# Optimization experiments

Hardware: AMD Instinct MI355X
Metric: run time of the kernel (lower is better)

The kernel has to match this reference:

```python
import jax, jax.numpy as jnp
import numpy as np

B, DIM, H, W = 64, 384, 28, 28
NH, HD, WS, SS = 6, 64, 7, 3
HID = 1536
N = WS * WS
NW = (H // WS) * (W // WS)
SCALE = HD ** -0.25  # qk_scale=None -> head_dim ** -0.25, applied to both q and k
EPS = 1e-5


def _rel_pos_index(ws):
    coords = np.stack(np.meshgrid(np.arange(ws), np.arange(ws), indexing='ij'))  # (2,ws,ws)
    flat = coords.reshape(2, -1)
    rel = (flat[:, :, None] - flat[:, None, :]).transpose(1, 2, 0).copy()  # (N,N,2)
    rel[..., 0] += ws - 1
    rel[..., 1] += ws - 1
    rel[..., 0] *= 2 * ws - 1
    return rel.sum(-1)  # (N,N) int


def _attn_mask(h, w, ws, ss):
    img = np.zeros((h, w))
    cnt = 0
    for hs in (slice(0, -ws), slice(-ws, -ss), slice(-ss, None)):
        for wsl in (slice(0, -ws), slice(-ws, -ss), slice(-ss, None)):
            img[hs, wsl] = cnt
            cnt += 1
    mw = img.reshape(h // ws, ws, w // ws, ws).transpose(0, 2, 1, 3).reshape(-1, ws * ws)  # (nW,N)
    diff = mw[:, None, :] - mw[:, :, None]
    return np.where(diff != 0, -100.0, 0.0).astype(np.float32)  # (nW,N,N)


REL_IDX = jnp.asarray(_rel_pos_index(WS))          # (N,N)
MASK = jnp.asarray(_attn_mask(H, W, WS, SS))       # (NW,N,N)


def _layernorm_bchw(x, w, b):
    mean = jnp.mean(x, axis=1, keepdims=True)
    var = jnp.var(x, axis=1, keepdims=True, ddof=1)  # torch.var_mean is unbiased
    return (x - mean) / jnp.sqrt(var + EPS) * w + b


def setup_inputs() -> dict:
    key = jax.random.key(0)
    ks = jax.random.split(key, 6)
    return {
        'x': jax.random.normal(ks[0], (B, DIM, H, W), jnp.float32),
        'norm1_w': jnp.ones((1, DIM, 1, 1), jnp.float32),
        'norm1_b': jnp.zeros((1, DIM, 1, 1), jnp.float32),
        'qkv_w': jax.random.normal(ks[1], (3 * NH * HD, DIM), jnp.float32) * 0.02,
        'rel_bias_table': jax.random.normal(ks[2], ((2 * WS - 1) ** 2, NH), jnp.float32) * 0.02,
        'proj_w': jax.random.normal(ks[3], (DIM, NH * HD), jnp.float32) * 0.02,
        'norm2_w': jnp.ones((1, DIM, 1, 1), jnp.float32),
        'norm2_b': jnp.zeros((1, DIM, 1, 1), jnp.float32),
        'mlp_w1': jax.random.normal(ks[4], (HID, DIM), jnp.float32) * 0.02,
        'mlp_w3': jax.random.normal(ks[5], (DIM, HID), jnp.float32) * 0.02,
    }


def reference(x, norm1_w, norm1_b, qkv_w, rel_bias_table, proj_w, norm2_w, norm2_b, mlp_w1, mlp_w3):
    b = x.shape[0]
    shortcut = x
    xn = _layernorm_bchw(x, norm1_w, norm1_b)
    xs = jnp.roll(xn, (-SS, -SS), axis=(2, 3))
    # window partition: (B,C,H,W) -> (B*nW, C, WS, WS)
    xw = xs.reshape(b, DIM, H // WS, WS, W // WS, WS).transpose(0, 2, 4, 1, 3, 5).reshape(-1, DIM, WS, WS)
    bw = xw.shape[0]
    # 1x1-conv qkv projection (no bias), then split heads
    qkv = jnp.einsum('oc,bchw->bohw', qkv_w, xw).reshape(bw, 3, NH, HD, N)
    q, k, v = jnp.moveaxis(qkv, 1, 0)  # each (bw, NH, HD, N)
    attn = jnp.einsum('bhdn,bhdm->bhnm', q * SCALE, k * SCALE)  # (bw,NH,N,N)
    bias = rel_bias_table[REL_IDX.reshape(-1)].reshape(N, N, NH).transpose(2, 0, 1)  # (NH,N,N)
    attn = attn + bias[None]
    attn = attn.reshape(b, NW, NH, N, N) + MASK[None, :, None]
    attn = jax.nn.softmax(attn.reshape(bw, NH, N, N), axis=-1)
    out = jnp.einsum('bhnm,bhdm->bhdn', attn, v)  # (bw,NH,HD,N)
    out = out.reshape(bw, NH * HD, WS, WS)
    out = jnp.einsum('oc,bchw->bohw', proj_w, out)
    # window reverse + unshift
    xr = out.reshape(b, H // WS, W // WS, DIM, WS, WS).transpose(0, 3, 1, 4, 2, 5).reshape(b, DIM, H, W)
    xr = jnp.roll(xr, (SS, SS), axis=(2, 3))
    x = shortcut + xr
    # conv MLP (1x1 convs, no bias, exact GELU)
    xn2 = _layernorm_bchw(x, norm2_w, norm2_b)
    h = jax.nn.gelu(jnp.einsum('oc,bchw->bohw', mlp_w1, xn2), approximate=False)
    x = x + jnp.einsum('oc,bchw->bohw', mlp_w3, h)
    return x
```

## Files before the change

kernel.cpp:

```cpp
#include <hip/hip_runtime.h>
#include <hip/hip_bf16.h>


typedef __bf16 bf16x8 __attribute__((ext_vector_type(8)));
typedef __bf16 bf16x4 __attribute__((ext_vector_type(4)));
typedef float  f32x4  __attribute__((ext_vector_type(4)));
typedef float  f32x2  __attribute__((ext_vector_type(2)));
typedef int    i32x4  __attribute__((ext_vector_type(4)));
typedef int    i32x2  __attribute__((ext_vector_type(2)));

#define GAS __attribute__((address_space(1)))
#define LAS __attribute__((address_space(3)))

#if __has_builtin(__builtin_amdgcn_cvt_pk_f32_fp8) && __has_builtin(__builtin_amdgcn_cvt_pk_fp8_f32)
#define HAS_HW_FP8 1
#else
#define HAS_HW_FP8 0
#endif

__device__ __forceinline__ int div7u(int m) { return (m * 37) >> 8; }

#if !HAS_HW_FP8
__device__ __forceinline__ float fp8_dec1(unsigned u) {
  unsigned s = (u >> 7) & 1, e = (u >> 3) & 15, m = u & 7;
  float nrm = __uint_as_float((s << 31) | ((e + 120) << 23) | (m << 20));
  float sub = (s ? -1.f : 1.f) * (float)m * 0.001953125f;
  return e ? nrm : sub;
}
__device__ __forceinline__ unsigned fp8_enc1(float f) {
  f = fminf(fmaxf(f, -448.f), 448.f);
  unsigned u = __float_as_uint(f);
  unsigned s = u >> 31;
  int e8 = (int)((u >> 23) & 255) - 120;
  unsigned m32 = u & 0x7fffff;
  if (e8 <= 0) return s << 7;
  unsigned m = m32 >> 20;
  unsigned rem = m32 & 0xfffff;
  m += (rem > 0x80000u) || (rem == 0x80000u && (m & 1));
  if (m == 8) { m = 0; ++e8; }
  if (e8 > 15 || (e8 == 15 && m == 7)) { e8 = 15; m = 6; }
  return (s << 7) | ((unsigned)e8 << 3) | m;
}
#endif

template <bool HI>
__device__ __forceinline__ f32x2 fp8_cvt2(int w) {
#if HAS_HW_FP8
  return __builtin_amdgcn_cvt_pk_f32_fp8(w, HI);
#else
  unsigned b0 = (w >> (HI ? 16 : 0)) & 255, b1 = (w >> (HI ? 24 : 8)) & 255;
  return (f32x2){fp8_dec1(b0), fp8_dec1(b1)};
#endif
}
template <bool HI>
__device__ __forceinline__ int fp8_pk2(float a, float b, int old) {
#if HAS_HW_FP8
  return __builtin_amdgcn_cvt_pk_fp8_f32(a, b, old, HI);
#else
  unsigned v = fp8_enc1(a) | (fp8_enc1(b) << 8);
  return HI ? (int)(((unsigned)old & 0xffffu) | (v << 16))
            : (int)(((unsigned)old & 0xffff0000u) | v);
#endif
}
__device__ __forceinline__ i32x4 fp8x8_to_bf16x8(i32x2 v) {
  f32x2 a = fp8_cvt2<false>(v[0]), b = fp8_cvt2<true>(v[0]);
  f32x2 c = fp8_cvt2<false>(v[1]), d = fp8_cvt2<true>(v[1]);
  bf16x8 r = {(__bf16)a[0], (__bf16)a[1], (__bf16)b[0], (__bf16)b[1],
              (__bf16)c[0], (__bf16)c[1], (__bf16)d[0], (__bf16)d[1]};
  return __builtin_bit_cast(i32x4, r);
}

__device__ __forceinline__ float gelu_f(float v) {
  float u = v * __builtin_fmaf(0.0356774f, v * v, 0.79788456f);
  float e = __expf(2.f * u);
  float t = 1.f - 2.f * __builtin_amdgcn_rcpf(e + 1.f);
  return 0.5f * v * (1.f + t);
}

__global__ __launch_bounds__(256) void cvt_all_kernel(const float* __restrict__ s0,
                                                      const float* __restrict__ s1,
                                                      const float* __restrict__ s2,
                                                      const float* __restrict__ s3,
                                                      __bf16* __restrict__ d0,
                                                      __bf16* __restrict__ d1,
                                                      __bf16* __restrict__ d2,
                                                      __bf16* __restrict__ d3,
                                                      const float* __restrict__ tbl,
                                                      float* __restrict__ be) {
  int i = blockIdx.x * 256 + threadIdx.x;
  if (i < 442368) { d0[i] = (__bf16)s0[i]; return; }
  i -= 442368;
  if (i < 147456) { d1[i] = (__bf16)s1[i]; return; }
  i -= 147456;
  if (i < 589824) { d2[i] = (__bf16)s2[i]; return; }
  i -= 589824;
  if (i < 589824) { d3[i] = (__bf16)s3[i]; return; }
  i -= 589824;
  if (i < 6 * 64 * 64) {
    int m = i & 63, n = (i >> 6) & 63, h = i >> 12;
    float v = 0.f;
    if (m < 49 && n < 49) {
      int in_ = div7u(n), jn = n - in_ * 7;
      int im  = div7u(m), jm = m - im * 7;
      v = tbl[((in_ - im + 6) * 13 + (jn - jm + 6)) * 6 + h];
    }
    be[i] = v;
  }
}

__global__ __launch_bounds__(256) void ln_t_kernel(const float* __restrict__ x,
                                                   const float* __restrict__ gw,
                                                   const float* __restrict__ gb,
                                                   __bf16* __restrict__ out) {
  __shared__ f32x4 ps[16][16], ps2[16][16];
  __shared__ __align__(16) __bf16 tile[64][198];
  const int tid = threadIdx.x;
  const int lane = tid & 63, w = tid >> 6;
  const int gq = lane & 15;
  const int sub = (w << 2) + (lane >> 4);
  const int tok0 = blockIdx.x << 6;
  const int tokg4 = tok0 + (gq << 2);
  const unsigned b = (unsigned)tokg4 / 784u;
  const unsigned p = (unsigned)tokg4 - b * 784u;
  const float* xp = x + (size_t)b * 301056u + p;

  f32x4 vals[24];
  f32x4 s4 = {0.f, 0.f, 0.f, 0.f}, s24 = {0.f, 0.f, 0.f, 0.f};
  #pragma unroll
  for (int half = 0; half < 2; ++half)
    #pragma unroll
    for (int k = 0; k < 12; ++k) {
      int c = half * 192 + sub * 12 + k;
      f32x4 v = *(const f32x4*)(xp + (size_t)c * 784u);
      vals[half * 12 + k] = v;
      s4 += v;
      s24 += v * v;
    }
  ps[sub][gq] = s4;
  ps2[sub][gq] = s24;
  __syncthreads();
  f32x4 S = {0.f, 0.f, 0.f, 0.f}, S2 = {0.f, 0.f, 0.f, 0.f};
  #pragma unroll
  for (int i = 0; i < 16; ++i) { S += ps[i][gq]; S2 += ps2[i][gq]; }
  f32x4 mean = S * (1.f / 384.f);
  f32x4 var = (S2 - S * mean) * (1.f / 383.f);
  f32x4 rstd;
  #pragma unroll
  for (int j = 0; j < 4; ++j) rstd[j] = rsqrtf(var[j] + 1e-5f);

  #pragma unroll
  for (int half = 0; half < 2; ++half) {
    if (half) __syncthreads();
    #pragma unroll
    for (int k = 0; k < 12; ++k) {
      int c = half * 192 + sub * 12 + k;
      float wgt = gw[c], bia = gb[c];
      f32x4 v = (vals[half * 12 + k] - mean) * rstd * wgt + bia;
      #pragma unroll
      for (int j = 0; j < 4; ++j)
        tile[(gq << 2) + j][sub * 12 + k] = (__bf16)v[j];
    }
    __syncthreads();
    #pragma unroll
    for (int it = 0; it < 6; ++it) {
      int idx = (it << 8) + tid;
      int row = idx / 24, colc = idx - row * 24;
      bf16x8 vv = *(const bf16x8*)(&tile[row][colc << 3]);
      *(bf16x8*)(out + (size_t)(tok0 + row) * 384 + half * 192 + (colc << 3)) = vv;
    }
  }
}

template <int EPI, int F8>
__global__ __launch_bounds__(256, 3) void gemm_bt(const __bf16* __restrict__ A, int lda,
                                                  const void* __restrict__ BtV, int ldb,
                                                  int K, int My,
                                                  void* __restrict__ outT, int ldo, int ocol,
                                                  float* __restrict__ outR,
                                                  const float* __restrict__ resid,
                                                  int tok_off) {
  constexpr bool B8 = (F8 && EPI == 2);
  constexpr int esz = B8 ? 1 : 2;
  __shared__ __align__(16) char smem[33792];
  const int tid = threadIdx.x;
  const int lane = tid & 63;
  const int w = tid >> 6;
  const int wr = w >> 1, wc = w & 1;
  const int c = lane & 15, g = lane >> 4;

  const int nwg = gridDim.x;
  const int orig = blockIdx.x;
  const int q = nwg >> 3, r = nwg & 7;
  const int xcd = orig & 7, ii = orig >> 3;
  const int wgid = (xcd < r ? xcd * (q + 1) : r * (q + 1) + (xcd - r) * q) + ii;
  const int bx = wgid / My;
  const int by = wgid - bx * My;
  const int m0 = by << 7;
  const int n0 = bx << 7;

  const __bf16* ap[4];
  const unsigned char* bp[4];
  #pragma unroll
  for (int i = 0; i < 4; ++i) {
    int s = (i << 8) + tid;
    int row = s >> 3;
    int kk = ((s ^ row) & 7) << 3;
    ap[i] = A + (size_t)(m0 + row) * lda + kk;
    bp[i] = (const unsigned char*)BtV + ((size_t)(n0 + row) * ldb + kk) * esz;
  }

  i32x4 sA0, sA1, sA2, sA3;
  i32x4 sB0, sB1, sB2, sB3;
  i32x2 t0, t1, t2, t3;
  auto issue = [&](int k0) {
    sA0 = *(const i32x4*)(ap[0] + k0);
    sA1 = *(const i32x4*)(ap[1] + k0);
    sA2 = *(const i32x4*)(ap[2] + k0);
    sA3 = *(const i32x4*)(ap[3] + k0);
    if constexpr (B8) {
      t0 = *(const i32x2*)(bp[0] + k0);
      t1 = *(const i32x2*)(bp[1] + k0);
      t2 = *(const i32x2*)(bp[2] + k0);
      t3 = *(const i32x2*)(bp[3] + k0);
    } else {
      sB0 = *(const i32x4*)(bp[0] + k0 * 2);
      sB1 = *(const i32x4*)(bp[1] + k0 * 2);
      sB2 = *(const i32x4*)(bp[2] + k0 * 2);
      sB3 = *(const i32x4*)(bp[3] + k0 * 2);
    }
  };
  auto write_lds = [&]() {
    *(i32x4*)(smem +         (((0 << 8) + tid) << 4)) = sA0;
    *(i32x4*)(smem +         (((1 << 8) + tid) << 4)) = sA1;
    *(i32x4*)(smem +         (((2 << 8) + tid) << 4)) = sA2;
    *(i32x4*)(smem +         (((3 << 8) + tid) << 4)) = sA3;
    if constexpr (B8) {
      *(i32x4*)(smem + 16384 + (((0 << 8) + tid) << 4)) = fp8x8_to_bf16x8(t0);
      *(i32x4*)(smem + 16384 + (((1 << 8) + tid) << 4)) = fp8x8_to_bf16x8(t1);
      *(i32x4*)(smem + 16384 + (((2 << 8) + tid) << 4)) = fp8x8_to_bf16x8(t2);
      *(i32x4*)(smem + 16384 + (((3 << 8) + tid) << 4)) = fp8x8_to_bf16x8(t3);
    } else {
      *(i32x4*)(smem + 16384 + (((0 << 8) + tid) << 4)) = sB0;
      *(i32x4*)(smem + 16384 + (((1 << 8) + tid) << 4)) = sB1;
      *(i32x4*)(smem + 16384 + (((2 << 8) + tid) << 4)) = sB2;
      *(i32x4*)(smem + 16384 + (((3 << 8) + tid) << 4)) = sB3;
    }
  };

  f32x4 acc[4][4] = {};
  const int nt = K >> 6;

  issue(0);
  write_lds();
  asm volatile("s_waitcnt lgkmcnt(0)" ::: "memory");
  __builtin_amdgcn_s_barrier();
  __builtin_amdgcn_sched_barrier(0);

  for (int t = 0; t < nt; ++t) {
    if (t + 1 < nt) issue((t + 1) << 6);
    const char* smA = smem;
    const char* smB = smem + 16384;
    #pragma unroll
    for (int ks = 0; ks < 2; ++ks) {
      bf16x8 af[4], bfv[4];
      #pragma unroll
      for (int mi = 0; mi < 4; ++mi) {
        int r2 = (wr << 6) + (mi << 4) + c;
        af[mi] = *(const bf16x8*)(smA + (r2 << 7) + (((ks << 6) + (g << 4)) ^ ((r2 & 7) << 4)));
      }
      #pragma unroll
      for (int nj = 0; nj < 4; ++nj) {
        int r2 = (wc << 6) + (nj << 4) + c;
        bfv[nj] = *(const bf16x8*)(smB + (r2 << 7) + (((ks << 6) + (g << 4)) ^ ((r2 & 7) << 4)));
      }
      #pragma unroll
      for (int mi = 0; mi < 4; ++mi)
        #pragma unroll
        for (int nj = 0; nj < 4; ++nj) {
          if constexpr (EPI == 2)
            acc[mi][nj] = __builtin_amdgcn_mfma_f32_16x16x32_bf16(bfv[nj], af[mi], acc[mi][nj], 0, 0, 0);
          else
            acc[mi][nj] = __builtin_amdgcn_mfma_f32_16x16x32_bf16(af[mi], bfv[nj], acc[mi][nj], 0, 0, 0);
        }
    }
    __builtin_amdgcn_s_barrier();
    if (t + 1 < nt) {
      write_lds();
      asm volatile("s_waitcnt lgkmcnt(0)" ::: "memory");
    }
    __builtin_amdgcn_s_barrier();
    __builtin_amdgcn_sched_barrier(0);
  }

  if constexpr (EPI <= 1) {
    #pragma unroll
    for (int mi = 0; mi < 4; ++mi)
      #pragma unroll
      for (int nj = 0; nj < 4; ++nj) {
        f32x4 v = acc[mi][nj];
        if constexpr (EPI == 1) {
          #pragma unroll
          for (int r2 = 0; r2 < 4; ++r2) v[r2] = gelu_f(v[r2]);
        }
        bf16x4 pk = {(__bf16)v[0], (__bf16)v[1], (__bf16)v[2], (__bf16)v[3]};
        int nl = (wc << 6) + (nj << 4) + c;
        int ml = (wr << 6) + (mi << 4) + (g << 2);
        *(bf16x4*)(smem + nl * 264 + ml * 2) = pk;
      }
    __syncthreads();
    #pragma unroll
    for (int it = 0; it < 8; ++it) {
      int id = (it << 8) + tid;
      int n = id >> 4, mc = id & 15;
      bf16x8 v = *(const bf16x8*)(smem + n * 264 + (mc << 4));
      if constexpr (F8) {
        int w0 = 0, w1 = 0;
        w0 = fp8_pk2<false>((float)v[0], (float)v[1], w0);
        w0 = fp8_pk2<true>((float)v[2], (float)v[3], w0);
        w1 = fp8_pk2<false>((float)v[4], (float)v[5], w1);
        w1 = fp8_pk2<true>((float)v[6], (float)v[7], w1);
        *(i32x2*)((unsigned char*)outT + (size_t)(n0 + n) * ldo + (ocol + m0 + (mc << 3))) =
            (i32x2){w0, w1};
      } else {
        *(bf16x8*)((__bf16*)outT + (size_t)(n0 + n) * ldo + (ocol + m0 + (mc << 3))) = v;
      }
    }
  } else {
    #pragma unroll
    for (int nj = 0; nj < 4; ++nj) {
      int tokb = tok_off + n0 + (wc << 6) + (nj << 4) + (g << 2);
      unsigned bb = (unsigned)tokb / 784u;
      unsigned pp = (unsigned)tokb - bb * 784u;
      size_t base2 = (size_t)bb * (384u * 784u) + pp;
      #pragma unroll
      for (int mi = 0; mi < 4; ++mi) {
        int o = m0 + (wr << 6) + (mi << 4) + c;
        size_t a2 = base2 + (size_t)o * 784u;
        f32x4 rv = *(const f32x4*)(resid + a2);
        f32x4 v = acc[mi][nj] + rv;
        *(f32x4*)(outR + a2) = v;
      }
    }
  }
}

__global__ __launch_bounds__(256, 2) void attn_kernel(const __bf16* __restrict__ qkv,
                                                      const float* __restrict__ be,
                                                      __bf16* __restrict__ outt) {
  __shared__ __align__(16) char smem_all[4][16384];
  const int tid = threadIdx.x;
  const int lane = tid & 63;
  const int w = tid >> 6;
  char* sm = (char*)smem_all[w];
  const int pair = blockIdx.x * 4 + w;
  const int h = pair % 6;
  const int wg = pair / 6;
  const int b = wg >> 4;
  const int wi = wg & 15;
  const int wh = wi >> 2, wwi = wi & 3;
  const int cc = lane & 15, g = lane >> 4;

  {
    int rsub = lane >> 3;
    int slot = lane & 7;
    int dc = (slot ^ rsub) << 3;
    #pragma unroll
    for (int i = 0; i < 8; ++i) {
      int r = i * 8 + rsub;
      int m = r < 49 ? r : 48;
      int im = div7u(m), jm = m - im * 7;
      int sh = wh * 7 + im + 3; if (sh >= 28) sh -= 28;
      int sw = wwi * 7 + jm + 3; if (sw >= 28) sw -= 28;
      size_t trow = (size_t)(b * 784 + sh * 28 + sw) * 1152;
      __builtin_amdgcn_global_load_lds((const GAS void*)(qkv + trow + 384 + h * 64 + dc),
                                       (LAS void*)(sm + i * 1024), 16, 0, 0);
      __builtin_amdgcn_global_load_lds((const GAS void*)(qkv + trow + h * 64 + dc),
                                       (LAS void*)(sm + 8192 + i * 1024), 16, 0, 0);
    }
  }
  asm volatile("s_waitcnt vmcnt(0)" ::: "memory");
  __syncthreads();

  f32x4 sacc[4][4] = {};
  #pragma unroll
  for (int ks = 0; ks < 2; ++ks) {
    bf16x8 kf[4], qf[4];
    #pragma unroll
    for (int mi = 0; mi < 4; ++mi) {
      int r = (mi << 4) + cc;
      kf[mi] = *(const bf16x8*)(sm + (r << 7) + (((ks << 6) + (g << 4)) ^ ((r & 7) << 4)));
    }
    #pragma unroll
    for (int nj = 0; nj < 4; ++nj) {
      int r = (nj << 4) + cc;
      qf[nj] = *(const bf16x8*)(sm + 8192 + (r << 7) + (((ks << 6) + (g << 4)) ^ ((r & 7) << 4)));
    }
    #pragma unroll
    for (int mi = 0; mi < 4; ++mi)
      #pragma unroll
      for (int nj = 0; nj < 4; ++nj)
        sacc[mi][nj] = __builtin_amdgcn_mfma_f32_16x16x32_bf16(kf[mi], qf[nj], sacc[mi][nj], 0, 0, 0);
  }
  __syncthreads();

  int r9m[4][4];
  #pragma unroll
  for (int mi = 0; mi < 4; ++mi)
    #pragma unroll
    for (int rr = 0; rr < 4; ++rr) {
      int m = (mi << 4) + (g << 2) + rr; if (m > 48) m = 48;
      int im = div7u(m), jm = m - im * 7;
      int sh = wh * 7 + im, sw = wwi * 7 + jm;
      r9m[mi][rr] = ((sh < 21) ? 0 : (sh < 25 ? 1 : 2)) * 3 + ((sw < 21) ? 0 : (sw < 25 ? 1 : 2));
    }

  #pragma unroll
  for (int nj = 0; nj < 4; ++nj) {
    int n = (nj << 4) + cc;
    int ncl = n > 48 ? 48 : n;
    int in_ = div7u(ncl), jn = ncl - in_ * 7;
    int shn = wh * 7 + in_, swn = wwi * 7 + jn;
    int r9n = ((shn < 21) ? 0 : (shn < 25 ? 1 : 2)) * 3 + ((swn < 21) ? 0 : (swn < 25 ? 1 : 2));
    float mx = -1e30f;
    #pragma unroll
    for (int mi = 0; mi < 4; ++mi) {
      f32x4 bia = *(const f32x4*)(be + (((h << 6) + n) << 6) + (mi << 4) + (g << 2));
      #pragma unroll
      for (int rr = 0; rr < 4; ++rr) {
        int m = (mi << 4) + (g << 2) + rr;
        float t = (m < 49)
            ? sacc[mi][nj][rr] * 0.125f + bia[rr] + ((r9m[mi][rr] == r9n) ? 0.f : -100.f)
            : -1e30f;
        sacc[mi][nj][rr] = t;
        mx = fmaxf(mx, t);
      }
    }
    mx = fmaxf(mx, __shfl_xor(mx, 16, 64));
    mx = fmaxf(mx, __shfl_xor(mx, 32, 64));
    float sum = 0.f;
    #pragma unroll
    for (int mi = 0; mi < 4; ++mi)
      #pragma unroll
      for (int rr = 0; rr < 4; ++rr) {
        float e = __expf(sacc[mi][nj][rr] - mx);
        sacc[mi][nj][rr] = e;
        sum += e;
      }
    sum += __shfl_xor(sum, 16, 64);
    sum += __shfl_xor(sum, 32, 64);
    float inv = __builtin_amdgcn_rcpf(sum);
    #pragma unroll
    for (int mi = 0; mi < 4; ++mi) {
      bf16x4 pk = {(__bf16)(sacc[mi][nj][0] * inv), (__bf16)(sacc[mi][nj][1] * inv),
                   (__bf16)(sacc[mi][nj][2] * inv), (__bf16)(sacc[mi][nj][3] * inv)};
      *(bf16x4*)(sm + 8192 + (n << 7) + (((mi << 5) + (g << 3)) ^ ((n & 7) << 4))) = pk;
    }
  }

  {
    int ml = lane & 15, dq = lane >> 4;
    #pragma unroll
    for (int it = 0; it < 4; ++it) {
      int m = (it << 4) + ml;
      int mc_ = m > 48 ? 48 : m;
      int im = div7u(mc_), jm = mc_ - im * 7;
      int sh = wh * 7 + im + 3; if (sh >= 28) sh -= 28;
      int sw = wwi * 7 + jm + 3; if (sw >= 28) sw -= 28;
      const __bf16* gv = qkv + (size_t)(b * 784 + sh * 28 + sw) * 1152 + 768 + h * 64;
      #pragma unroll
      for (int hd = 0; hd < 2; ++hd) {
        int dbase = (hd << 5) + (dq << 3);
        bf16x8 v = *(const bf16x8*)(gv + dbase);
        #pragma unroll
        for (int j = 0; j < 8; ++j) {
          int d = dbase + j;
          *(__bf16*)(sm + (d << 7) + ((((m >> 3) ^ (d & 7)) << 4) + ((m & 7) << 1))) = v[j];
        }
      }
    }
  }
  __syncthreads();

  f32x4 oacc[4][4] = {};
  #pragma unroll
  for (int ks = 0; ks < 2; ++ks) {
    bf16x8 pf[4], vf[4];
    #pragma unroll
    for (int ni = 0; ni < 4; ++ni) {
      int n = (ni << 4) + cc;
      pf[ni] = *(const bf16x8*)(sm + 8192 + (n << 7) + (((ks << 6) + (g << 4)) ^ ((n & 7) << 4)));
    }
    #pragma unroll
    for (int dj = 0; dj < 4; ++dj) {
      int d = (dj << 4) + cc;
      vf[dj] = *(const bf16x8*)(sm + (d << 7) + ((((ks << 2) + g) ^ (d & 7)) << 4));
    }
    #pragma unroll
    for (int ni = 0; ni < 4; ++ni)
      #pragma unroll
      for (int dj = 0; dj < 4; ++dj)
        oacc[ni][dj] = __builtin_amdgcn_mfma_f32_16x16x32_bf16(pf[ni], vf[dj], oacc[ni][dj], 0, 0, 0);
  }

  #pragma unroll
  for (int ni = 0; ni < 4; ++ni)
    #pragma unroll
    for (int rr = 0; rr < 4; ++rr) {
      int n = (ni << 4) + (g << 2) + rr;
      if (n < 49) {
        int im = div7u(n), jn = n - im * 7;
        int sh = wh * 7 + im + 3; if (sh >= 28) sh -= 28;
        int sw = wwi * 7 + jn + 3; if (sw >= 28) sw -= 28;
        __bf16* op = outt + (size_t)(b * 784 + sh * 28 + sw) * 384 + h * 64;
        #pragma unroll
        for (int dj = 0; dj < 4; ++dj)
          op[(dj << 4) + cc] = (__bf16)oacc[ni][dj][rr];
      }
    }
}

extern "C" void kernel_launch(void* const* d_in, const int* in_sizes, int n_in,
                              void* d_out, int out_size, void* d_ws, size_t ws_size,
                              hipStream_t stream) {
  (void)in_sizes; (void)n_in; (void)out_size; (void)ws_size;
  const float* x     = (const float*)d_in[0];
  const float* n1w   = (const float*)d_in[1];
  const float* n1b   = (const float*)d_in[2];
  const float* qkvw  = (const float*)d_in[3];
  const float* tbl   = (const float*)d_in[4];
  const float* projw = (const float*)d_in[5];
  const float* n2w   = (const float*)d_in[6];
  const float* n2b   = (const float*)d_in[7];
  const float* w1    = (const float*)d_in[8];
  const float* w3    = (const float*)d_in[9];
  float* out = (float*)d_out;

  char* ws = (char*)d_ws;
  __bf16* bufA = (__bf16*)ws;
  __bf16* bufB = (__bf16*)(ws + 38535168);
  float*  be   = (float*)(ws + 154140672);
  __bf16* wq   = (__bf16*)(ws + 154238976);
  __bf16* wp   = wq + 442368;
  __bf16* wm1  = wp + 147456;
  __bf16* wm3  = wm1 + 589824;

  cvt_all_kernel<<<7008, 256, 0, stream>>>(qkvw, projw, w1, w3, wq, wp, wm1, wm3, tbl, be);

  ln_t_kernel<<<784, 256, 0, stream>>>(x, n1w, n1b, bufA);
  gemm_bt<0, 0><<<392 * 9, 256, 0, stream>>>(wq, 384, bufA, 384, 384, 9,
                                             bufB, 1152, 0, nullptr, nullptr, 0);
  attn_kernel<<<1536, 256, 0, stream>>>(bufB, be, bufA);
  gemm_bt<2, 0><<<392 * 3, 256, 0, stream>>>(wp, 384, bufA, 384, 384, 3,
                                             nullptr, 0, 0, out, x, 0);
  ln_t_kernel<<<784, 256, 0, stream>>>(out, n2w, n2b, bufA);
  unsigned char* h8 = (unsigned char*)bufB;
  for (int hh = 0; hh < 2; ++hh) {
    const int toff = hh * 25088;
    gemm_bt<1, 1><<<196 * 12, 256, 0, stream>>>(wm1, 384, bufA + (size_t)toff * 384, 384, 384, 12,
                                                (void*)h8, 1536, 0, nullptr, nullptr, 0);
    gemm_bt<2, 1><<<196 * 3, 256, 0, stream>>>(wm3, 1536, (const void*)h8, 1536, 1536, 3,
                                               nullptr, 0, 0, out, out, toff);
  }
}
```

Before: 392.5 us.

## Add LDS-free direct-load GEMM with 128x256 tiles for qkv and MLP1

```diff
diff --git a/kernel.cpp b/kernel.cpp
--- a/kernel.cpp
+++ b/kernel.cpp
@@ -171,16 +171,95 @@
   }
 }
 
-template <int EPI, int F8>
+template <int EPI>
+__global__ __launch_bounds__(256, 2) void gemm_l2(const __bf16* __restrict__ A,
+                                                  const __bf16* __restrict__ Bt, int ldb,
+                                                  int My,
+                                                  void* __restrict__ outT, int ldo) {
+  __shared__ __align__(16) char smem[67584];
+  const int tid = threadIdx.x;
+  const int lane = tid & 63;
+  const int w = tid >> 6;
+  const int wr = w >> 1, wc = w & 1;
+  const int c = lane & 15, g = lane >> 4;
+
+  const int nwg = gridDim.x;
+  const int orig = blockIdx.x;
+  const int q = nwg >> 3, r = nwg & 7;
+  const int xcd = orig & 7, ii = orig >> 3;
+  const int wgid = (xcd < r ? xcd * (q + 1) : r * (q + 1) + (xcd - r) * q) + ii;
+  const int bx = wgid / My;
+  const int by = wgid - bx * My;
+  const int m0 = by << 7;
+  const int n0 = bx << 8;
+
+  const __bf16* aP = A + (size_t)(m0 + (wr << 6) + c) * 384 + (g << 3);
+  const __bf16* bP = Bt + (size_t)(n0 + (wc << 7) + c) * ldb + (g << 3);
+
+  f32x4 acc[4][8];
+  #pragma unroll
+  for (int mi = 0; mi < 4; ++mi)
+    #pragma unroll
+    for (int nj = 0; nj < 8; ++nj) acc[mi][nj] = (f32x4){0.f, 0.f, 0.f, 0.f};
+
+  #pragma unroll
+  for (int kk = 0; kk < 12; ++kk) {
+    bf16x8 af[4], bfv[8];
+    #pragma unroll
+    for (int mi = 0; mi < 4; ++mi)
+      af[mi] = *(const bf16x8*)(aP + (mi << 4) * 384 + (kk << 5));
+    #pragma unroll
+    for (int nj = 0; nj < 8; ++nj)
+      bfv[nj] = *(const bf16x8*)(bP + (size_t)((nj << 4)) * ldb + (kk << 5));
+    #pragma unroll
+    for (int mi = 0; mi < 4; ++mi)
+      #pragma unroll
+      for (int nj = 0; nj < 8; ++nj)
+        acc[mi][nj] = __builtin_amdgcn_mfma_f32_16x16x32_bf16(af[mi], bfv[nj], acc[mi][nj], 0, 0, 0);
+  }
+
+  #pragma unroll
+  for (int mi = 0; mi < 4; ++mi)
+    #pragma unroll
+    for (int nj = 0; nj < 8; ++nj) {
+      f32x4 v = acc[mi][nj];
+      if constexpr (EPI == 1) {
+        #pragma unroll
+        for (int j = 0; j < 4; ++j) v[j] = gelu_f(v[j]);
+      }
+      bf16x4 pk = {(__bf16)v[0], (__bf16)v[1], (__bf16)v[2], (__bf16)v[3]};
+      int tok = (wc << 7) + (nj << 4) + c;
+      int ml = (wr << 6) + (mi << 4) + (g << 2);
+      *(bf16x4*)(smem + tok * 264 + ml * 2) = pk;
+    }
+  __syncthreads();
+  #pragma unroll
+  for (int it = 0; it < 16; ++it) {
+    int id = (it << 8) + tid;
+    int n = id >> 4, mc = id & 15;
+    bf16x8 v = *(const bf16x8*)(smem + n * 264 + (mc << 4));
+    if constexpr (EPI == 1) {
+      int w0 = 0, w1 = 0;
+      w0 = fp8_pk2<false>((float)v[0], (float)v[1], w0);
+      w0 = fp8_pk2<true>((float)v[2], (float)v[3], w0);
+      w1 = fp8_pk2<false>((float)v[4], (float)v[5], w1);
+      w1 = fp8_pk2<true>((float)v[6], (float)v[7], w1);
+      *(i32x2*)((unsigned char*)outT + (size_t)(n0 + n) * ldo + (m0 + (mc << 3))) =
+          (i32x2){w0, w1};
+    } else {
+      *(bf16x8*)((__bf16*)outT + (size_t)(n0 + n) * ldo + (m0 + (mc << 3))) = v;
+    }
+  }
+}
+
+template <int F8>
 __global__ __launch_bounds__(256, 3) void gemm_bt(const __bf16* __restrict__ A, int lda,
                                                   const void* __restrict__ BtV, int ldb,
                                                   int K, int My,
-                                                  void* __restrict__ outT, int ldo, int ocol,
                                                   float* __restrict__ outR,
                                                   const float* __restrict__ resid,
                                                   int tok_off) {
-  constexpr bool B8 = (F8 && EPI == 2);
-  constexpr int esz = B8 ? 1 : 2;
+  constexpr int esz = F8 ? 1 : 2;
   __shared__ __align__(16) char smem[33792];
   const int tid = threadIdx.x;
   const int lane = tid & 63;
@@ -217,7 +296,7 @@
     sA1 = *(const i32x4*)(ap[1] + k0);
     sA2 = *(const i32x4*)(ap[2] + k0);
     sA3 = *(const i32x4*)(ap[3] + k0);
-    if constexpr (B8) {
+    if constexpr (F8) {
       t0 = *(const i32x2*)(bp[0] + k0);
       t1 = *(const i32x2*)(bp[1] + k0);
       t2 = *(const i32x2*)(bp[2] + k0);
@@ -234,7 +313,7 @@
     *(i32x4*)(smem +         (((1 << 8) + tid) << 4)) = sA1;
     *(i32x4*)(smem +         (((2 << 8) + tid) << 4)) = sA2;
     *(i32x4*)(smem +         (((3 << 8) + tid) << 4)) = sA3;
-    if constexpr (B8) {
+    if constexpr (F8) {
       *(i32x4*)(smem + 16384 + (((0 << 8) + tid) << 4)) = fp8x8_to_bf16x8(t0);
       *(i32x4*)(smem + 16384 + (((1 << 8) + tid) << 4)) = fp8x8_to_bf16x8(t1);
       *(i32x4*)(smem + 16384 + (((2 << 8) + tid) << 4)) = fp8x8_to_bf16x8(t2);
@@ -276,12 +355,8 @@
       #pragma unroll
       for (int mi = 0; mi < 4; ++mi)
         #pragma unroll
-        for (int nj = 0; nj < 4; ++nj) {
-          if constexpr (EPI == 2)
-            acc[mi][nj] = __builtin_amdgcn_mfma_f32_16x16x32_bf16(bfv[nj], af[mi], acc[mi][nj], 0, 0, 0);
-          else
-            acc[mi][nj] = __builtin_amdgcn_mfma_f32_16x16x32_bf16(af[mi], bfv[nj], acc[mi][nj], 0, 0, 0);
-        }
+        for (int nj = 0; nj < 4; ++nj)
+          acc[mi][nj] = __builtin_amdgcn_mfma_f32_16x16x32_bf16(bfv[nj], af[mi], acc[mi][nj], 0, 0, 0);
     }
     __builtin_amdgcn_s_barrier();
     if (t + 1 < nt) {
@@ -292,54 +367,19 @@
     __builtin_amdgcn_sched_barrier(0);
   }
 
-  if constexpr (EPI <= 1) {
-    #pragma unroll
-    for (int mi = 0; mi < 4; ++mi)
-      #pragma unroll
-      for (int nj = 0; nj < 4; ++nj) {
-        f32x4 v = acc[mi][nj];
-        if constexpr (EPI == 1) {
-          #pragma unroll
-          for (int r2 = 0; r2 < 4; ++r2) v[r2] = gelu_f(v[r2]);
-        }
-        bf16x4 pk = {(__bf16)v[0], (__bf16)v[1], (__bf16)v[2], (__bf16)v[3]};
-        int nl = (wc << 6) + (nj << 4) + c;
-        int ml = (wr << 6) + (mi << 4) + (g << 2);
-        *(bf16x4*)(smem + nl * 264 + ml * 2) = pk;
-      }
-    __syncthreads();
-    #pragma unroll
-    for (int it = 0; it < 8; ++it) {
-      int id = (it << 8) + tid;
-      int n = id >> 4, mc = id & 15;
-      bf16x8 v = *(const bf16x8*)(smem + n * 264 + (mc << 4));
-      if constexpr (F8) {
-        int w0 = 0, w1 = 0;
-        w0 = fp8_pk2<false>((float)v[0], (float)v[1], w0);
-        w0 = fp8_pk2<true>((float)v[2], (float)v[3], w0);
-        w1 = fp8_pk2<false>((float)v[4], (float)v[5], w1);
-        w1 = fp8_pk2<true>((float)v[6], (float)v[7], w1);
-        *(i32x2*)((unsigned char*)outT + (size_t)(n0 + n) * ldo + (ocol + m0 + (mc << 3))) =
-            (i32x2){w0, w1};
-      } else {
-        *(bf16x8*)((__bf16*)outT + (size_t)(n0 + n) * ldo + (ocol + m0 + (mc << 3))) = v;
-      }
-    }
-  } else {
-    #pragma unroll
-    for (int nj = 0; nj < 4; ++nj) {
-      int tokb = tok_off + n0 + (wc << 6) + (nj << 4) + (g << 2);
-      unsigned bb = (unsigned)tokb / 784u;
-      unsigned pp = (unsigned)tokb - bb * 784u;
-      size_t base2 = (size_t)bb * (384u * 784u) + pp;
-      #pragma unroll
-      for (int mi = 0; mi < 4; ++mi) {
-        int o = m0 + (wr << 6) + (mi << 4) + c;
-        size_t a2 = base2 + (size_t)o * 784u;
-        f32x4 rv = *(const f32x4*)(resid + a2);
-        f32x4 v = acc[mi][nj] + rv;
-        *(f32x4*)(outR + a2) = v;
-      }
+  #pragma unroll
+  for (int nj = 0; nj < 4; ++nj) {
+    int tokb = tok_off + n0 + (wc << 6) + (nj << 4) + (g << 2);
+    unsigned bb = (unsigned)tokb / 784u;
+    unsigned pp = (unsigned)tokb - bb * 784u;
+    size_t base2 = (size_t)bb * (384u * 784u) + pp;
+    #pragma unroll
+    for (int mi = 0; mi < 4; ++mi) {
+      int o = m0 + (wr << 6) + (mi << 4) + c;
+      size_t a2 = base2 + (size_t)o * 784u;
+      f32x4 rv = *(const f32x4*)(resid + a2);
+      f32x4 v = acc[mi][nj] + rv;
+      *(f32x4*)(outR + a2) = v;
     }
   }
 }
@@ -547,18 +587,16 @@
   cvt_all_kernel<<<7008, 256, 0, stream>>>(qkvw, projw, w1, w3, wq, wp, wm1, wm3, tbl, be);
 
   ln_t_kernel<<<784, 256, 0, stream>>>(x, n1w, n1b, bufA);
-  gemm_bt<0, 0><<<392 * 9, 256, 0, stream>>>(wq, 384, bufA, 384, 384, 9,
-                                             bufB, 1152, 0, nullptr, nullptr, 0);
+  gemm_l2<0><<<9 * 196, 256, 0, stream>>>(wq, bufA, 384, 9, bufB, 1152);
   attn_kernel<<<1536, 256, 0, stream>>>(bufB, be, bufA);
-  gemm_bt<2, 0><<<392 * 3, 256, 0, stream>>>(wp, 384, bufA, 384, 384, 3,
-                                             nullptr, 0, 0, out, x, 0);
+  gemm_bt<0><<<392 * 3, 256, 0, stream>>>(wp, 384, bufA, 384, 384, 3, out, x, 0);
   ln_t_kernel<<<784, 256, 0, stream>>>(out, n2w, n2b, bufA);
   unsigned char* h8 = (unsigned char*)bufB;
   for (int hh = 0; hh < 2; ++hh) {
     const int toff = hh * 25088;
-    gemm_bt<1, 1><<<196 * 12, 256, 0, stream>>>(wm1, 384, bufA + (size_t)toff * 384, 384, 384, 12,
-                                                (void*)h8, 1536, 0, nullptr, nullptr, 0);
-    gemm_bt<2, 1><<<196 * 3, 256, 0, stream>>>(wm3, 1536, (const void*)h8, 1536, 1536, 3,
-                                               nullptr, 0, 0, out, out, toff);
-  }
-}
+    gemm_l2<1><<<12 * 98, 256, 0, stream>>>(wm1, bufA + (size_t)toff * 384, 384, 12,
+                                            (void*)h8, 1536);
+    gemm_bt<1><<<196 * 3, 256, 0, stream>>>(wm3, 1536, (const void*)h8, 1536, 1536, 3,
+                                            out, out, toff);
+  }
+}
```

New measurement: 552.0 us. +40.7%, slower.

## Store intermediate residual in bf16 and run MLP GEMMs in single launches

Applied to the files above, without the earlier changes.

```diff
diff --git a/kernel.cpp b/kernel.cpp
--- a/kernel.cpp
+++ b/kernel.cpp
@@ -108,7 +108,8 @@
   }
 }
 
-__global__ __launch_bounds__(256) void ln_t_kernel(const float* __restrict__ x,
+template <typename TIN>
+__global__ __launch_bounds__(256) void ln_t_kernel(const TIN* __restrict__ x,
                                                    const float* __restrict__ gw,
                                                    const float* __restrict__ gb,
                                                    __bf16* __restrict__ out) {
@@ -122,7 +123,7 @@
   const int tokg4 = tok0 + (gq << 2);
   const unsigned b = (unsigned)tokg4 / 784u;
   const unsigned p = (unsigned)tokg4 - b * 784u;
-  const float* xp = x + (size_t)b * 301056u + p;
+  const TIN* xp = x + (size_t)b * 301056u + p;
 
   f32x4 vals[24];
   f32x4 s4 = {0.f, 0.f, 0.f, 0.f}, s24 = {0.f, 0.f, 0.f, 0.f};
@@ -131,7 +132,13 @@
     #pragma unroll
     for (int k = 0; k < 12; ++k) {
       int c = half * 192 + sub * 12 + k;
-      f32x4 v = *(const f32x4*)(xp + (size_t)c * 784u);
+      f32x4 v;
+      if constexpr (sizeof(TIN) == 4) {
+        v = *(const f32x4*)(xp + (size_t)c * 784u);
+      } else {
+        bf16x4 t = *(const bf16x4*)(xp + (size_t)c * 784u);
+        v = (f32x4){(float)t[0], (float)t[1], (float)t[2], (float)t[3]};
+      }
       vals[half * 12 + k] = v;
       s4 += v;
       s24 += v * v;
@@ -176,10 +183,10 @@
                                                   const void* __restrict__ BtV, int ldb,
                                                   int K, int My,
                                                   void* __restrict__ outT, int ldo, int ocol,
-                                                  float* __restrict__ outR,
-                                                  const float* __restrict__ resid,
+                                                  void* __restrict__ outR,
+                                                  const void* __restrict__ resid,
                                                   int tok_off) {
-  constexpr bool B8 = (F8 && EPI == 2);
+  constexpr bool B8 = (F8 && EPI >= 2);
   constexpr int esz = B8 ? 1 : 2;
   __shared__ __align__(16) char smem[33792];
   const int tid = threadIdx.x;
@@ -277,7 +284,7 @@
       for (int mi = 0; mi < 4; ++mi)
         #pragma unroll
         for (int nj = 0; nj < 4; ++nj) {
-          if constexpr (EPI == 2)
+          if constexpr (EPI >= 2)
             acc[mi][nj] = __builtin_amdgcn_mfma_f32_16x16x32_bf16(bfv[nj], af[mi], acc[mi][nj], 0, 0, 0);
           else
             acc[mi][nj] = __builtin_amdgcn_mfma_f32_16x16x32_bf16(af[mi], bfv[nj], acc[mi][nj], 0, 0, 0);
@@ -336,9 +343,18 @@
       for (int mi = 0; mi < 4; ++mi) {
         int o = m0 + (wr << 6) + (mi << 4) + c;
         size_t a2 = base2 + (size_t)o * 784u;
-        f32x4 rv = *(const f32x4*)(resid + a2);
-        f32x4 v = acc[mi][nj] + rv;
-        *(f32x4*)(outR + a2) = v;
+        if constexpr (EPI == 2) {
+          bf16x4 rv = *(const bf16x4*)((const __bf16*)resid + a2);
+          f32x4 v;
+          #pragma unroll
+          for (int j = 0; j < 4; ++j) v[j] = acc[mi][nj][j] + (float)rv[j];
+          *(f32x4*)((float*)outR + a2) = v;
+        } else {
+          f32x4 rv = *(const f32x4*)((const float*)resid + a2);
+          f32x4 v = acc[mi][nj] + rv;
+          bf16x4 pk = {(__bf16)v[0], (__bf16)v[1], (__bf16)v[2], (__bf16)v[3]};
+          *(bf16x4*)((__bf16*)outR + a2) = pk;
+        }
       }
     }
   }
@@ -537,7 +553,8 @@
 
   char* ws = (char*)d_ws;
   __bf16* bufA = (__bf16*)ws;
-  __bf16* bufB = (__bf16*)(ws + 38535168);
+  unsigned char* h8 = (unsigned char*)(ws + 38535168);
+  __bf16* x2b = (__bf16*)(ws + 38535168 + 77070336);
   float*  be   = (float*)(ws + 154140672);
   __bf16* wq   = (__bf16*)(ws + 154238976);
   __bf16* wp   = wq + 442368;
@@ -546,19 +563,15 @@
 
   cvt_all_kernel<<<7008, 256, 0, stream>>>(qkvw, projw, w1, w3, wq, wp, wm1, wm3, tbl, be);
 
-  ln_t_kernel<<<784, 256, 0, stream>>>(x, n1w, n1b, bufA);
+  ln_t_kernel<float><<<784, 256, 0, stream>>>(x, n1w, n1b, bufA);
   gemm_bt<0, 0><<<392 * 9, 256, 0, stream>>>(wq, 384, bufA, 384, 384, 9,
-                                             bufB, 1152, 0, nullptr, nullptr, 0);
-  attn_kernel<<<1536, 256, 0, stream>>>(bufB, be, bufA);
-  gemm_bt<2, 0><<<392 * 3, 256, 0, stream>>>(wp, 384, bufA, 384, 384, 3,
-                                             nullptr, 0, 0, out, x, 0);
-  ln_t_kernel<<<784, 256, 0, stream>>>(out, n2w, n2b, bufA);
-  unsigned char* h8 = (unsigned char*)bufB;
-  for (int hh = 0; hh < 2; ++hh) {
-    const int toff = hh * 25088;
-    gemm_bt<1, 1><<<196 * 12, 256, 0, stream>>>(wm1, 384, bufA + (size_t)toff * 384, 384, 384, 12,
-                                                (void*)h8, 1536, 0, nullptr, nullptr, 0);
-    gemm_bt<2, 1><<<196 * 3, 256, 0, stream>>>(wm3, 1536, (const void*)h8, 1536, 1536, 3,
-                                               nullptr, 0, 0, out, out, toff);
-  }
-}
+                                             (void*)h8, 1152, 0, nullptr, nullptr, 0);
+  attn_kernel<<<1536, 256, 0, stream>>>((const __bf16*)h8, be, bufA);
+  gemm_bt<3, 0><<<392 * 3, 256, 0, stream>>>(wp, 384, bufA, 384, 384, 3,
+                                             nullptr, 0, 0, (void*)x2b, x, 0);
+  ln_t_kernel<__bf16><<<784, 256, 0, stream>>>(x2b, n2w, n2b, bufA);
+  gemm_bt<1, 1><<<392 * 12, 256, 0, stream>>>(wm1, 384, bufA, 384, 384, 12,
+                                              (void*)h8, 1536, 0, nullptr, nullptr, 0);
+  gemm_bt<2, 1><<<392 * 3, 256, 0, stream>>>(wm3, 1536, (const void*)h8, 1536, 1536, 3,
+                                             nullptr, 0, 0, out, x2b, 0);
+}
```

Result: faster. 344.8 us (-12.2%).
